# Performance work log

Hardware: AMD Instinct MI355X
Metric: run time of the kernel (lower is better)

Reference implementation:

```python
import jax, jax.numpy as jnp
import numpy as np

N_NODES = 50000
N_EDGES = 800000
N_RELS = 16
D = 128


def _rgcn_layer(h, W, b, loop_w, gate_w, src, dst, rel, norm, apply_relu, n_nodes):
    # Transform all node features by every relation weight once: [R, N, D_out].
    # Equivalent to DGL bmm_maybe_select's per-edge W[rel] bmm, but avoids an
    # [E, D, D] gather of weights.
    h_all = jnp.einsum('nd,rde->rne', h, W)
    msg = h_all[rel, src]                                    # [E, D_out]
    msg = msg * norm                                         # edge norm scaling
    gate_logit = jnp.einsum('nd,rd->rn', h, gate_w[..., 0])  # [R, N]
    gate = jax.nn.sigmoid(gate_logit[rel, src])[:, None]     # [E, 1]
    msg = msg * gate
    agg = jax.ops.segment_sum(msg, dst, num_segments=n_nodes)  # fn.sum -> dst
    out = agg + b + h @ loop_w                               # bias + self loop
    if apply_relu:
        out = jax.nn.relu(out)
    return out  # dropout is identity in eval mode


def setup_inputs() -> dict:
    key = jax.random.key(0)
    ks = jax.random.split(key, 12)
    gain = float(np.sqrt(2.0))  # relu gain (xavier-ish scale; values arbitrary)
    def xav(k, shape):
        fan = shape[-2] + shape[-1]
        s = gain * np.sqrt(6.0 / fan)
        return jax.random.uniform(k, shape, jnp.float32, -s, s)
    return {
        'h': jax.random.normal(ks[0], (N_NODES, D), jnp.float32),
        'norm': jax.random.uniform(ks[1], (N_EDGES, 1), jnp.float32),
        'weight0': xav(ks[2], (N_RELS, D, D)),
        'bias0': jnp.zeros((D,), jnp.float32),
        'loop_w0': xav(ks[3], (D, D)),
        'gate_w0': xav(ks[4], (N_RELS, D, 1)),
        'weight1': xav(ks[5], (N_RELS, D, D)),
        'bias1': jnp.zeros((D,), jnp.float32),
        'loop_w1': xav(ks[6], (D, D)),
        'gate_w1': xav(ks[7], (N_RELS, D, 1)),
        'src': jax.random.randint(ks[8], (N_EDGES,), 0, N_NODES, jnp.int32),
        'dst': jax.random.randint(ks[9], (N_EDGES,), 0, N_NODES, jnp.int32),
        'rel_type': jax.random.randint(ks[10], (N_EDGES,), 0, N_RELS, jnp.int32),
    }


def reference(h, norm, weight0, bias0, loop_w0, gate_w0,
              weight1, bias1, loop_w1, gate_w1, src, dst, rel_type):
    n_nodes = h.shape[0]
    # Layer 0: activation=relu (idx < num_hidden_layers - 1)
    h = _rgcn_layer(h, weight0, bias0, loop_w0, gate_w0, src, dst, rel_type,
                    norm, True, n_nodes)
    # Layer 1: no activation
    h = _rgcn_layer(h, weight1, bias1, loop_w1, gate_w1, src, dst, rel_type,
                    norm, False, n_nodes)
    return h
```

## Files before the change

### kernel.cpp

```cpp
#include <hip/hip_runtime.h>
#include <hip/hip_bf16.h>
#include <stdint.h>

#define NN 50000
#define NE 800000
#define NR 16
#define NP (NN * NR)
#define NB1 ((NP + 255) / 256)
#define NTILES ((NN + 127) / 128)

typedef unsigned short u16;
typedef unsigned int u32;

typedef __bf16 bf16x8 __attribute__((ext_vector_type(8)));
typedef __bf16 bf16x2 __attribute__((ext_vector_type(2)));
typedef float f32x4 __attribute__((ext_vector_type(4)));

__device__ __forceinline__ u16 f2bf(float f) {
  u32 u = __float_as_uint(f);
  u = u + 0x7FFFu + ((u >> 16) & 1u);
  return (u16)(u >> 16);
}

__device__ __forceinline__ u32 pk2bf(float x, float y) {
#if __has_builtin(__builtin_amdgcn_cvt_pk_bf16_f32)
  bf16x2 r = __builtin_amdgcn_cvt_pk_bf16_f32(x, y);
  union { bf16x2 v; u32 u; } c;
  c.v = r;
  return c.u;
#else
  return (u32)f2bf(x) | ((u32)f2bf(y) << 16);
#endif
}

__device__ __forceinline__ float bflo(u32 w) { return __uint_as_float(w << 16); }
__device__ __forceinline__ float bfhi(u32 w) { return __uint_as_float(w & 0xFFFF0000u); }

__global__ void hist_kernel(const int* __restrict__ dst, const int* __restrict__ rel,
                            int* __restrict__ counts) {
  int e = blockIdx.x * 256 + threadIdx.x;
  if (e < NE) atomicAdd(&counts[dst[e] * NR + rel[e]], 1);
}

__global__ void scan_partial(const int* __restrict__ counts, int* __restrict__ bsum) {
  __shared__ int buf[256];
  int t = threadIdx.x;
  int i = blockIdx.x * 256 + t;
  int v = (i < NP) ? counts[i] : 0;
  buf[t] = v;
  __syncthreads();
  for (int off = 1; off < 256; off <<= 1) {
    int x = buf[t];
    int y = (t >= off) ? buf[t - off] : 0;
    __syncthreads();
    buf[t] = x + y;
    __syncthreads();
  }
  if (t == 255) bsum[blockIdx.x] = buf[255];
}

__global__ void scan_mid(const int* __restrict__ bsum, int* __restrict__ boff,
                         int* __restrict__ total_out) {
  __shared__ int buf[1024];
  int t = threadIdx.x;
  int v[4];
  int sum = 0;
#pragma unroll
  for (int i = 0; i < 4; ++i) {
    int idx = t * 4 + i;
    v[i] = (idx < NB1) ? bsum[idx] : 0;
    sum += v[i];
  }
  buf[t] = sum;
  __syncthreads();
  for (int off = 1; off < 1024; off <<= 1) {
    int x = buf[t];
    int y = (t >= off) ? buf[t - off] : 0;
    __syncthreads();
    buf[t] = x + y;
    __syncthreads();
  }
  int excl = buf[t] - sum;
#pragma unroll
  for (int i = 0; i < 4; ++i) {
    int idx = t * 4 + i;
    if (idx < NB1) { boff[idx] = excl; excl += v[i]; }
  }
  if (t == 1023) *total_out = buf[1023];
}

__global__ void scan_final(const int* __restrict__ counts, const int* __restrict__ boff,
                           int* __restrict__ starts, int* __restrict__ cursor) {
  __shared__ int buf[256];
  int t = threadIdx.x;
  int i = blockIdx.x * 256 + t;
  int v = (i < NP) ? counts[i] : 0;
  buf[t] = v;
  __syncthreads();
  for (int off = 1; off < 256; off <<= 1) {
    int x = buf[t];
    int y = (t >= off) ? buf[t - off] : 0;
    __syncthreads();
    buf[t] = x + y;
    __syncthreads();
  }
  int s = boff[blockIdx.x] + buf[t] - v;
  if (i < NP) {
    starts[i] = s;
    cursor[i] = s;
  }
}

__global__ void scatter_kernel(const int* __restrict__ src, const int* __restrict__ dst,
                               const int* __restrict__ rel, const float* __restrict__ norm,
                               int* __restrict__ cursor, uint2* __restrict__ esd) {
  int e = blockIdx.x * 256 + threadIdx.x;
  if (e < NE) {
    int r = rel[e];
    int pos = atomicAdd(&cursor[dst[e] * NR + r], 1);
    esd[pos] = make_uint2(((u32)r << 16) | (u32)src[e], __float_as_uint(norm[e]));
  }
}

__global__ void convert_wt(const float* __restrict__ w0, const float* __restrict__ lw0,
                           const float* __restrict__ w1, const float* __restrict__ lw1,
                           u16* __restrict__ Wt) {
  int m = blockIdx.y;
  int idx = blockIdx.x * 256 + threadIdx.x;
  int d = idx >> 7, k = idx & 127;
  const float* s;
  if (m < 16) s = w0 + (size_t)m * 16384;
  else if (m == 16) s = lw0;
  else if (m < 33) s = w1 + (size_t)(m - 17) * 16384;
  else s = lw1;
  Wt[(size_t)m * 16384 + idx] = f2bf(s[k * 128 + d]);
}

__global__ void hconv_kernel(const float* __restrict__ h, u16* __restrict__ hbf) {
  int i = blockIdx.x * 256 + threadIdx.x;
  float4 v = ((const float4*)h)[i];
  ushort4 u;
  u.x = f2bf(v.x); u.y = f2bf(v.y); u.z = f2bf(v.z); u.w = f2bf(v.w);
  ((ushort4*)hbf)[i] = u;
}

__global__ void gates_kernel(const u16* __restrict__ hbf, const float* __restrict__ gw,
                             float* __restrict__ gates) {
  __shared__ float hs[16 * 132];
  __shared__ float gws[16 * 132];
  int t = threadIdx.x;
  int n0 = blockIdx.x * 16;
#pragma unroll
  for (int i = 0; i < 2; ++i) {
    int f = t + 256 * i;
    int row = f >> 5, c4 = (f & 31) * 4;
    ushort4 u = *(const ushort4*)&hbf[(size_t)(n0 + row) * 128 + c4];
    hs[row * 132 + c4 + 0] = __uint_as_float((u32)u.x << 16);
    hs[row * 132 + c4 + 1] = __uint_as_float((u32)u.y << 16);
    hs[row * 132 + c4 + 2] = __uint_as_float((u32)u.z << 16);
    hs[row * 132 + c4 + 3] = __uint_as_float((u32)u.w << 16);
    *(float4*)&gws[row * 132 + c4] = *(const float4*)&gw[row * 128 + c4];
  }
  __syncthreads();
  int nl = t >> 4, r = t & 15;
  float s = 0.f;
#pragma unroll 8
  for (int k = 0; k < 128; ++k) s += hs[nl * 132 + k] * gws[r * 132 + k];
  gates[r * NN + n0 + nl] = 1.f / (1.f + __expf(-s));
}

__global__ __launch_bounds__(256)
void aggregate_kernel(const u32* __restrict__ hbf32, const uint2* __restrict__ esd,
                      const float* __restrict__ gates, const int* __restrict__ starts,
                      u32* __restrict__ agg) {
  int wave = threadIdx.x >> 6, lane = threadIdx.x & 63;
  int v = blockIdx.x * 4 + wave;
  if (v >= NN) return;
  int s = starts[v * NR];
  int e = starts[v * NR + NR];
  u32* aggp = agg + (size_t)v * 64 + lane;
  float a0 = 0.f, a1 = 0.f;
  int cur = 0;
  int j = s;
  for (; j + 8 <= e; j += 8) {
    uint2 p[8];
#pragma unroll
    for (int i = 0; i < 8; ++i) p[i] = esd[j + i];
    u32 w[8];
    float gt[8];
#pragma unroll
    for (int i = 0; i < 8; ++i) {
      u32 rs = p[i].x;
      u32 sn = rs & 0xFFFFu;
      w[i] = hbf32[sn * 64u + (u32)lane];
      gt[i] = gates[(rs >> 16) * (u32)NN + sn];
    }
#pragma unroll
    for (int i = 0; i < 8; ++i) {
      int rel = (int)(p[i].x >> 16);
      while (cur < rel) {
        aggp[(size_t)cur * NN * 64] = pk2bf(a0, a1);
        a0 = 0.f; a1 = 0.f;
        ++cur;
      }
      float coef = gt[i] * __uint_as_float(p[i].y);
      a0 = fmaf(coef, bflo(w[i]), a0);
      a1 = fmaf(coef, bfhi(w[i]), a1);
    }
  }
  for (; j < e; ++j) {
    uint2 p = esd[j];
    u32 rs = p.x;
    u32 sn = rs & 0xFFFFu;
    int rel = (int)(rs >> 16);
    while (cur < rel) {
      aggp[(size_t)cur * NN * 64] = pk2bf(a0, a1);
      a0 = 0.f; a1 = 0.f;
      ++cur;
    }
    float coef = gates[(u32)rel * (u32)NN + sn] * __uint_as_float(p.y);
    u32 w = hbf32[sn * 64u + (u32)lane];
    a0 = fmaf(coef, bflo(w), a0);
    a1 = fmaf(coef, bfhi(w), a1);
  }
  while (cur < NR) {
    aggp[(size_t)cur * NN * 64] = pk2bf(a0, a1);
    a0 = 0.f; a1 = 0.f;
    ++cur;
  }
}


#define REP8(X) X(0) X(1) X(2) X(3) X(4) X(5) X(6) X(7)

#define BG_ISSUE(i)                                                           \
  {                                                                           \
    int u8 = t + 256 * i;                                                     \
    int row = u8 >> 4, c8 = (u8 & 15) * 8;                                    \
    int n = n0 + row;                                                         \
    int nc = n < NN ? n : NN - 1;                                             \
    rw##i = *(const uint4*)&wbase[row * 128 + c8];                            \
    ra##i = *(const uint4*)&srcbase[(size_t)nc * 128 + c8];                   \
  }

#define BG_COMMIT(i)                                                          \
  {                                                                           \
    int u8 = t + 256 * i;                                                     \
    int row = u8 >> 4, c8 = (u8 & 15) * 8;                                    \
    *(uint4*)&As[row * 136 + c8] = ra##i;                                     \
    *(uint4*)&Ws[row * 136 + c8] = rw##i;                                     \
  }

#define BG_MFMA                                                               \
  _Pragma("unroll")                                                           \
  for (int kk = 0; kk < 4; ++kk) {                                            \
    int k0 = kk * 32 + quad * 8;                                              \
    bf16x8 fa[4], fb[4];                                                      \
    _Pragma("unroll")                                                         \
    for (int i2 = 0; i2 < 4; ++i2)                                            \
      fa[i2] = *(const bf16x8*)&Ws[(wd + i2 * 16 + mrow) * 136 + k0];         \
    _Pragma("unroll")                                                         \
    for (int j2 = 0; j2 < 4; ++j2)                                            \
      fb[j2] = *(const bf16x8*)&As[(wn + j2 * 16 + mrow) * 136 + k0];         \
    _Pragma("unroll")                                                         \
    for (int i2 = 0; i2 < 4; ++i2)                                            \
      _Pragma("unroll")                                                       \
      for (int j2 = 0; j2 < 4; ++j2)                                          \
        acc[i2][j2] =                                                         \
            __builtin_amdgcn_mfma_f32_16x16x32_bf16(fa[i2], fb[j2],           \
                                                    acc[i2][j2], 0, 0, 0);    \
  }

template <int LAYER>
__global__ __launch_bounds__(256, 2)
void biggemm_kernel(const u16* __restrict__ aggu, const u16* __restrict__ hbf,
                    const u16* __restrict__ Wt, const float* __restrict__ bias,
                    u16* __restrict__ hb_out, float* __restrict__ fout) {
  __shared__ u16 As[128 * 136];
  __shared__ u16 Ws[128 * 136];
  int t = threadIdx.x;
  int n0 = blockIdx.x * 128;
  int wave = t >> 6, lane = t & 63;
  int wd = (wave & 1) * 64, wn = (wave >> 1) * 64;
  int mrow = lane & 15, quad = lane >> 4;
  float4 bv[4];
#pragma unroll
  for (int i = 0; i < 4; ++i) bv[i] = *(const float4*)&bias[wd + i * 16 + quad * 4];
  f32x4 acc[4][4];
#pragma unroll
  for (int i = 0; i < 4; ++i)
#pragma unroll
    for (int j = 0; j < 4; ++j) acc[i][j] = (f32x4){0.f, 0.f, 0.f, 0.f};

  uint4 ra0, ra1, ra2, ra3, ra4, ra5, ra6, ra7;
  uint4 rw0, rw1, rw2, rw3, rw4, rw5, rw6, rw7;
  const u16* srcbase = aggu;
  const u16* wbase = Wt;
  REP8(BG_ISSUE)
  for (int m = 0; m < 16; ++m) {
    REP8(BG_COMMIT)
    __syncthreads();
    int mm = m + 1;
    srcbase = (mm < 16) ? aggu + (size_t)mm * NN * 128 : hbf;
    wbase = Wt + (size_t)mm * 16384;
    REP8(BG_ISSUE)
    BG_MFMA
    __syncthreads();
  }
  REP8(BG_COMMIT)
  __syncthreads();
  BG_MFMA

#pragma unroll
  for (int j = 0; j < 4; ++j) {
    int n = n0 + wn + j * 16 + mrow;
    if (n < NN) {
#pragma unroll
      for (int i = 0; i < 4; ++i) {
        int d0 = wd + i * 16 + quad * 4;
        float v0 = acc[i][j][0] + bv[i].x;
        float v1 = acc[i][j][1] + bv[i].y;
        float v2 = acc[i][j][2] + bv[i].z;
        float v3 = acc[i][j][3] + bv[i].w;
        if (LAYER == 0) {
          v0 = fmaxf(v0, 0.f); v1 = fmaxf(v1, 0.f);
          v2 = fmaxf(v2, 0.f); v3 = fmaxf(v3, 0.f);
          uint2 st;
          st.x = pk2bf(v0, v1);
          st.y = pk2bf(v2, v3);
          *(uint2*)&hb_out[(size_t)n * 128 + d0] = st;
        } else {
          float4 st = make_float4(v0, v1, v2, v3);
          *(float4*)&fout[(size_t)n * 128 + d0] = st;
        }
      }
    }
  }
}

extern "C" void kernel_launch(void* const* d_in, const int* in_sizes, int n_in,
                              void* d_out, int out_size, void* d_ws, size_t ws_size,
                              hipStream_t stream) {
  const float* h0   = (const float*)d_in[0];
  const float* norm = (const float*)d_in[1];
  const float* w0   = (const float*)d_in[2];
  const float* b0   = (const float*)d_in[3];
  const float* lw0  = (const float*)d_in[4];
  const float* gw0  = (const float*)d_in[5];
  const float* w1   = (const float*)d_in[6];
  const float* b1   = (const float*)d_in[7];
  const float* lw1  = (const float*)d_in[8];
  const float* gw1  = (const float*)d_in[9];
  const int*   src  = (const int*)d_in[10];
  const int*   dst  = (const int*)d_in[11];
  const int*   rel  = (const int*)d_in[12];
  float* out = (float*)d_out;

  char* p = (char*)d_ws;
  auto alloc = [&](size_t bytes) -> void* {
    void* q = (void*)p;
    p += (bytes + 255) & ~(size_t)255;
    return q;
  };
  u16*   Wt     = (u16*)alloc((size_t)34 * 16384 * 2);
  float* gates  = (float*)alloc((size_t)NR * NN * 4);
  u16*   hbf0   = (u16*)alloc((size_t)NN * 128 * 2);
  u16*   hbf1   = (u16*)alloc((size_t)NN * 128 * 2);
  int*   counts = (int*)alloc((size_t)NP * 4);
  int*   cursor = (int*)alloc((size_t)NP * 4);
  int*   starts = (int*)alloc((size_t)(NP + 1) * 4);
  int*   bsum   = (int*)alloc((size_t)NB1 * 4);
  int*   boff   = (int*)alloc((size_t)NB1 * 4);
  uint2* esd    = (uint2*)alloc((size_t)NE * 8);
  u32*   agg    = (u32*)alloc((size_t)NN * NR * 64 * 4);

  hipMemsetAsync(counts, 0, (size_t)NP * 4, stream);
  hist_kernel<<<NE / 256, 256, 0, stream>>>(dst, rel, counts);
  scan_partial<<<NB1, 256, 0, stream>>>(counts, bsum);
  scan_mid<<<1, 1024, 0, stream>>>(bsum, boff, starts + NP);
  scan_final<<<NB1, 256, 0, stream>>>(counts, boff, starts, cursor);
  scatter_kernel<<<NE / 256, 256, 0, stream>>>(src, dst, rel, norm, cursor, esd);
  convert_wt<<<dim3(64, 34), 256, 0, stream>>>(w0, lw0, w1, lw1, Wt);
  hconv_kernel<<<NN * 32 / 256, 256, 0, stream>>>(h0, hbf0);

  gates_kernel<<<NN / 16, 256, 0, stream>>>(hbf0, gw0, gates);
  aggregate_kernel<<<(NN + 3) / 4, 256, 0, stream>>>(
      (const u32*)hbf0, esd, gates, starts, agg);
  biggemm_kernel<0><<<NTILES, 256, 0, stream>>>(
      (const u16*)agg, hbf0, Wt, b0, hbf1, nullptr);

  gates_kernel<<<NN / 16, 256, 0, stream>>>(hbf1, gw1, gates);
  aggregate_kernel<<<(NN + 3) / 4, 256, 0, stream>>>(
      (const u32*)hbf1, esd, gates, starts, agg);
  biggemm_kernel<1><<<NTILES, 256, 0, stream>>>(
      (const u16*)agg, hbf1, Wt + (size_t)17 * 16384, b1, nullptr, out);
}
```

Baseline: 451.2 us.

## Fuse per-relation edge aggregation into the relation GEMM to drop agg buffer

The separate aggregate kernel, which wrote a [R,N,D] bf16 aggregate buffer, is removed. The GEMM kernel now computes each relation's gated, normed neighbor sum directly into shared memory per 128-node tile before the MFMA step, prefetching the first two edges per (node, relation) bin. This eliminates the large intermediate write and re-read (about 200MB per layer). In exchange the GEMM kernel now does irregular gather work with only 391 blocks, so parallelism is lower and gather latency may stall the MFMA pipeline.

```diff
diff --git a/kernel.cpp b/kernel.cpp
--- a/kernel.cpp
+++ b/kernel.cpp
@@ -169,85 +169,20 @@
   gates[r * NN + n0 + nl] = 1.f / (1.f + __expf(-s));
 }
 
-__global__ __launch_bounds__(256)
-void aggregate_kernel(const u32* __restrict__ hbf32, const uint2* __restrict__ esd,
-                      const float* __restrict__ gates, const int* __restrict__ starts,
-                      u32* __restrict__ agg) {
-  int wave = threadIdx.x >> 6, lane = threadIdx.x & 63;
-  int v = blockIdx.x * 4 + wave;
-  if (v >= NN) return;
-  int s = starts[v * NR];
-  int e = starts[v * NR + NR];
-  u32* aggp = agg + (size_t)v * 64 + lane;
-  float a0 = 0.f, a1 = 0.f;
-  int cur = 0;
-  int j = s;
-  for (; j + 8 <= e; j += 8) {
-    uint2 p[8];
-#pragma unroll
-    for (int i = 0; i < 8; ++i) p[i] = esd[j + i];
-    u32 w[8];
-    float gt[8];
-#pragma unroll
-    for (int i = 0; i < 8; ++i) {
-      u32 rs = p[i].x;
-      u32 sn = rs & 0xFFFFu;
-      w[i] = hbf32[sn * 64u + (u32)lane];
-      gt[i] = gates[(rs >> 16) * (u32)NN + sn];
-    }
-#pragma unroll
-    for (int i = 0; i < 8; ++i) {
-      int rel = (int)(p[i].x >> 16);
-      while (cur < rel) {
-        aggp[(size_t)cur * NN * 64] = pk2bf(a0, a1);
-        a0 = 0.f; a1 = 0.f;
-        ++cur;
-      }
-      float coef = gt[i] * __uint_as_float(p[i].y);
-      a0 = fmaf(coef, bflo(w[i]), a0);
-      a1 = fmaf(coef, bfhi(w[i]), a1);
-    }
-  }
-  for (; j < e; ++j) {
-    uint2 p = esd[j];
-    u32 rs = p.x;
-    u32 sn = rs & 0xFFFFu;
-    int rel = (int)(rs >> 16);
-    while (cur < rel) {
-      aggp[(size_t)cur * NN * 64] = pk2bf(a0, a1);
-      a0 = 0.f; a1 = 0.f;
-      ++cur;
-    }
-    float coef = gates[(u32)rel * (u32)NN + sn] * __uint_as_float(p.y);
-    u32 w = hbf32[sn * 64u + (u32)lane];
-    a0 = fmaf(coef, bflo(w), a0);
-    a1 = fmaf(coef, bfhi(w), a1);
-  }
-  while (cur < NR) {
-    aggp[(size_t)cur * NN * 64] = pk2bf(a0, a1);
-    a0 = 0.f; a1 = 0.f;
-    ++cur;
-  }
-}
-
 
 #define REP8(X) X(0) X(1) X(2) X(3) X(4) X(5) X(6) X(7)
 
-#define BG_ISSUE(i)                                                           \
+#define W_ISSUE(i)                                                            \
   {                                                                           \
     int u8 = t + 256 * i;                                                     \
     int row = u8 >> 4, c8 = (u8 & 15) * 8;                                    \
-    int n = n0 + row;                                                         \
-    int nc = n < NN ? n : NN - 1;                                             \
     rw##i = *(const uint4*)&wbase[row * 128 + c8];                            \
-    ra##i = *(const uint4*)&srcbase[(size_t)nc * 128 + c8];                   \
-  }
-
-#define BG_COMMIT(i)                                                          \
+  }
+
+#define W_COMMIT(i)                                                           \
   {                                                                           \
     int u8 = t + 256 * i;                                                     \
     int row = u8 >> 4, c8 = (u8 & 15) * 8;                                    \
-    *(uint4*)&As[row * 136 + c8] = ra##i;                                     \
     *(uint4*)&Ws[row * 136 + c8] = rw##i;                                     \
   }
 
@@ -273,16 +208,20 @@
 
 template <int LAYER>
 __global__ __launch_bounds__(256, 2)
-void biggemm_kernel(const u16* __restrict__ aggu, const u16* __restrict__ hbf,
-                    const u16* __restrict__ Wt, const float* __restrict__ bias,
-                    u16* __restrict__ hb_out, float* __restrict__ fout) {
+void fused_kernel(const u16* __restrict__ hbf, const uint2* __restrict__ esd,
+                  const float* __restrict__ gates, const int* __restrict__ starts,
+                  const u16* __restrict__ Wt, const float* __restrict__ bias,
+                  u16* __restrict__ hb_out, float* __restrict__ fout) {
+  const u32* hbf32 = (const u32*)hbf;
   __shared__ u16 As[128 * 136];
   __shared__ u16 Ws[128 * 136];
   int t = threadIdx.x;
   int n0 = blockIdx.x * 128;
-  int wave = t >> 6, lane = t & 63;
+  int lane = t & 63;
+  int wave = __builtin_amdgcn_readfirstlane(t >> 6);
   int wd = (wave & 1) * 64, wn = (wave >> 1) * 64;
   int mrow = lane & 15, quad = lane >> 4;
+  int wrow0 = wave * 32;
   float4 bv[4];
 #pragma unroll
   for (int i = 0; i < 4; ++i) bv[i] = *(const float4*)&bias[wd + i * 16 + quad * 4];
@@ -292,22 +231,84 @@
 #pragma unroll
     for (int j = 0; j < 4; ++j) acc[i][j] = (f32x4){0.f, 0.f, 0.f, 0.f};
 
-  uint4 ra0, ra1, ra2, ra3, ra4, ra5, ra6, ra7;
   uint4 rw0, rw1, rw2, rw3, rw4, rw5, rw6, rw7;
-  const u16* srcbase = aggu;
   const u16* wbase = Wt;
-  REP8(BG_ISSUE)
+  REP8(W_ISSUE)
   for (int m = 0; m < 16; ++m) {
-    REP8(BG_COMMIT)
-    __syncthreads();
-    int mm = m + 1;
-    srcbase = (mm < 16) ? aggu + (size_t)mm * NN * 128 : hbf;
-    wbase = Wt + (size_t)mm * 16384;
-    REP8(BG_ISSUE)
+#pragma unroll 1
+    for (int g = 0; g < 4; ++g) {
+      int vb = n0 + wrow0 + g * 8;
+      int s_[8], c_[8];
+#pragma unroll
+      for (int i = 0; i < 8; ++i) {
+        int v = vb + i;
+        int vc = v < NN ? v : NN - 1;
+        int bin = vc * 16 + m;
+        int s0 = starts[bin];
+        int e0 = starts[bin + 1];
+        s_[i] = s0;
+        c_[i] = v < NN ? e0 - s0 : 0;
+      }
+      uint2 p1[8], p2[8];
+      u32 h1[8], h2[8];
+      float g1[8], g2[8];
+#pragma unroll
+      for (int i = 0; i < 8; ++i) {
+        int e1 = s_[i] < NE ? s_[i] : NE - 1;
+        int e2 = s_[i] + 1 < NE ? s_[i] + 1 : NE - 1;
+        p1[i] = esd[e1];
+        p2[i] = esd[e2];
+      }
+#pragma unroll
+      for (int i = 0; i < 8; ++i) {
+        u32 sn1 = p1[i].x & 0xFFFFu;
+        u32 sn2 = p2[i].x & 0xFFFFu;
+        h1[i] = hbf32[sn1 * 64u + (u32)lane];
+        h2[i] = hbf32[sn2 * 64u + (u32)lane];
+        g1[i] = gates[(p1[i].x >> 16) * (u32)NN + sn1];
+        g2[i] = gates[(p2[i].x >> 16) * (u32)NN + sn2];
+      }
+#pragma unroll
+      for (int i = 0; i < 8; ++i) {
+        float a0 = 0.f, a1 = 0.f;
+        if (c_[i] >= 1) {
+          float coef = g1[i] * __uint_as_float(p1[i].y);
+          a0 = coef * bflo(h1[i]);
+          a1 = coef * bfhi(h1[i]);
+        }
+        if (c_[i] >= 2) {
+          float coef = g2[i] * __uint_as_float(p2[i].y);
+          a0 = fmaf(coef, bflo(h2[i]), a0);
+          a1 = fmaf(coef, bfhi(h2[i]), a1);
+        }
+        int jend = s_[i] + c_[i];
+        for (int j = s_[i] + 2; j < jend; ++j) {
+          uint2 p = esd[j];
+          u32 sn = p.x & 0xFFFFu;
+          float coef = gates[(p.x >> 16) * (u32)NN + sn] * __uint_as_float(p.y);
+          u32 hv = hbf32[sn * 64u + (u32)lane];
+          a0 = fmaf(coef, bflo(hv), a0);
+          a1 = fmaf(coef, bfhi(hv), a1);
+        }
+        *(u32*)&As[(wrow0 + g * 8 + i) * 136 + lane * 2] = pk2bf(a0, a1);
+      }
+    }
+    REP8(W_COMMIT)
+    __syncthreads();
+    wbase = Wt + (size_t)(m + 1) * 16384;
+    REP8(W_ISSUE)
     BG_MFMA
     __syncthreads();
   }
-  REP8(BG_COMMIT)
+#pragma unroll
+  for (int i = 0; i < 8; ++i) {
+    int u8 = t + 256 * i;
+    int row = u8 >> 4, c8 = (u8 & 15) * 8;
+    int n = n0 + row;
+    int nc = n < NN ? n : NN - 1;
+    *(uint4*)&As[row * 136 + c8] = *(const uint4*)&hbf[(size_t)nc * 128 + c8];
+  }
+  REP8(W_COMMIT)
   __syncthreads();
   BG_MFMA
 
@@ -372,7 +373,6 @@
   int*   bsum   = (int*)alloc((size_t)NB1 * 4);
   int*   boff   = (int*)alloc((size_t)NB1 * 4);
   uint2* esd    = (uint2*)alloc((size_t)NE * 8);
-  u32*   agg    = (u32*)alloc((size_t)NN * NR * 64 * 4);
 
   hipMemsetAsync(counts, 0, (size_t)NP * 4, stream);
   hist_kernel<<<NE / 256, 256, 0, stream>>>(dst, rel, counts);
@@ -384,14 +384,10 @@
   hconv_kernel<<<NN * 32 / 256, 256, 0, stream>>>(h0, hbf0);
 
   gates_kernel<<<NN / 16, 256, 0, stream>>>(hbf0, gw0, gates);
-  aggregate_kernel<<<(NN + 3) / 4, 256, 0, stream>>>(
-      (const u32*)hbf0, esd, gates, starts, agg);
-  biggemm_kernel<0><<<NTILES, 256, 0, stream>>>(
-      (const u16*)agg, hbf0, Wt, b0, hbf1, nullptr);
+  fused_kernel<0><<<NTILES, 256, 0, stream>>>(
+      hbf0, esd, gates, starts, Wt, b0, hbf1, nullptr);
 
   gates_kernel<<<NN / 16, 256, 0, stream>>>(hbf1, gw1, gates);
-  aggregate_kernel<<<(NN + 3) / 4, 256, 0, stream>>>(
-      (const u32*)hbf1, esd, gates, starts, agg);
-  biggemm_kernel<1><<<NTILES, 256, 0, stream>>>(
-      (const u16*)agg, hbf1, Wt + (size_t)17 * 16384, b1, nullptr, out);
-}
+  fused_kernel<1><<<NTILES, 256, 0, stream>>>(
+      hbf1, esd, gates, starts, Wt + (size_t)17 * 16384, b1, nullptr, out);
+}
```

After: 766.1 us. 1.7x slower.
